# Kernel tuning notes

Measured on AMD Instinct MI355X. Metric: run time of the kernel, lower is better.

Reference implementation:

```python
import jax, jax.numpy as jnp
import numpy as np
import math

D = 128      # d_model == num_filters
L = 4        # num_conv_layers
K = 7        # kernel_size
H = 8        # num_heads
B, S = 64, 400


def setup_inputs() -> dict:
    key = jax.random.key(0)
    ks = jax.random.split(key, 24)
    s = 0.02
    inp = {}
    inp['x'] = jax.random.normal(ks[0], (B, S, D), dtype=jnp.float32)
    # per-conv-layer params (stacked over L)
    inp['ln_g'] = jnp.ones((L, D), jnp.float32)
    inp['ln_b'] = jnp.zeros((L, D), jnp.float32)
    inp['dw_w'] = jax.random.normal(ks[1], (L, D, D, K), dtype=jnp.float32) * s
    inp['dw_b'] = jnp.zeros((L, D), jnp.float32)
    inp['pw_w'] = jax.random.normal(ks[2], (L, D, D), dtype=jnp.float32) * s
    inp['pw_b'] = jnp.zeros((L, D), jnp.float32)
    # attention block
    inp['attln_g'] = jnp.ones((D,), jnp.float32)
    inp['attln_b'] = jnp.zeros((D,), jnp.float32)
    inp['wq'] = jax.random.normal(ks[3], (D, D), dtype=jnp.float32) * s
    inp['bq'] = jnp.zeros((D,), jnp.float32)
    inp['wk'] = jax.random.normal(ks[4], (D, D), dtype=jnp.float32) * s
    inp['bk'] = jnp.zeros((D,), jnp.float32)
    inp['wv'] = jax.random.normal(ks[5], (D, D), dtype=jnp.float32) * s
    inp['bv'] = jnp.zeros((D,), jnp.float32)
    inp['wp'] = jax.random.normal(ks[6], (D, D), dtype=jnp.float32) * s
    inp['bp'] = jnp.zeros((D,), jnp.float32)
    # ffn
    inp['ffnln_g'] = jnp.ones((D,), jnp.float32)
    inp['ffnln_b'] = jnp.zeros((D,), jnp.float32)
    inp['fc_w'] = jax.random.normal(ks[7], (D, D), dtype=jnp.float32) * s
    inp['fc_b'] = jnp.zeros((D,), jnp.float32)
    return inp


def _layernorm(x, g, b, eps=1e-5):
    mu = jnp.mean(x, axis=-1, keepdims=True)
    var = jnp.var(x, axis=-1, keepdims=True)
    return (x - mu) * jax.lax.rsqrt(var + eps) * g + b


def _pos_encoding(seq_len, channels, dtype):
    pos = jnp.arange(seq_len, dtype=dtype)                       # [S]
    freq = 1.0 / (10000.0 ** (jnp.arange(0, channels, 2, dtype=dtype) / channels))
    sin_inp = pos[:, None] * freq[None, :]                       # [S, C/2]
    return jnp.concatenate([jnp.sin(sin_inp), jnp.cos(sin_inp)], axis=-1)  # [S, C]


def _encoder_fwd(x, ln_g, ln_b, dw_w, dw_b, pw_w, pw_b,
                 attln_g, attln_b, wq, bq, wk, bk, wv, bv, wp, bp,
                 ffnln_g, ffnln_b, fc_w, fc_b):
    b, s, d = x.shape
    out = x + _pos_encoding(s, d, x.dtype)[None, :, :]

    # conv stack: LN -> transpose -> (full) conv K -> pointwise conv -> transpose
    pad = dw_w.shape[-1] // 2
    for i in range(dw_w.shape[0]):
        h = _layernorm(out, ln_g[i], ln_b[i])
        t = jnp.transpose(h, (0, 2, 1))                          # [B, D, S]
        t = jax.lax.conv_general_dilated(
            t, dw_w[i], window_strides=(1,), padding=[(pad, pad)],
            dimension_numbers=('NCH', 'OIH', 'NCH')) + dw_b[i][None, :, None]
        t = jnp.einsum('bds,fd->bfs', t, pw_w[i]) + pw_b[i][None, :, None]
        out = jnp.transpose(t, (0, 2, 1))                        # [B, S, D]

    # causal self-attention (explicit scores, per original)
    h = _layernorm(out, attln_g, attln_b)
    hd = d // H
    q = (jnp.einsum('bsd,od->bso', h, wq) + bq).reshape(b, s, H, hd)
    k = (jnp.einsum('bsd,od->bso', h, wk) + bk).reshape(b, s, H, hd)
    v = (jnp.einsum('bsd,od->bso', h, wv) + bv).reshape(b, s, H, hd)
    att = jnp.einsum('bqhd,bkhd->bhqk', q, k) / math.sqrt(hd)    # [B, H, S, S]
    causal = jnp.tril(jnp.ones((s, s), dtype=bool))
    att = jnp.where(causal[None, None], att, jnp.asarray(-1e10, att.dtype))
    att = jax.nn.softmax(att, axis=-1)
    y = jnp.einsum('bhqk,bkhd->bqhd', att, v).reshape(b, s, d)
    y = jnp.einsum('bsd,od->bso', y, wp) + bp

    # ffn
    y = _layernorm(y, ffnln_g, ffnln_b)
    y = jnp.einsum('bsd,od->bso', y, fc_w) + fc_b
    return jax.nn.relu(y)


def reference(x, ln_g, ln_b, dw_w, dw_b, pw_w, pw_b,
              attln_g, attln_b, wq, bq, wk, bk, wv, bv, wp, bp,
              ffnln_g, ffnln_b, fc_w, fc_b):
    return _encoder_fwd(x, ln_g, ln_b, dw_w, dw_b, pw_w, pw_b,
                        attln_g, attln_b, wq, bq, wk, bk, wv, bv, wp, bp,
                        ffnln_g, ffnln_b, fc_w, fc_b)
```

## Files before the change

kernel.cpp:

```cpp
#include <hip/hip_runtime.h>
#include <hip/hip_bf16.h>
#include <math.h>

#define Dm 128
#define Lc 4
#define Kc 7
#define Hh 8
#define Bb 64
#define Ss 400
#define SsP 448
#define TOK (Bb*Ss)

typedef __attribute__((ext_vector_type(8))) short bf16x8;
typedef __attribute__((ext_vector_type(4))) float f32x4;

__device__ __forceinline__ float bf2f(unsigned int u) {
    union { unsigned int i; float f; } x; x.i = u << 16; return x.f;
}
__device__ __forceinline__ unsigned short f2bf(float f) {
    __hip_bfloat16 h = __float2bfloat16(f);
    return __builtin_bit_cast(unsigned short, h);
}
__device__ __forceinline__ unsigned int packbf(float a, float b) {
    return (unsigned int)f2bf(a) | ((unsigned int)f2bf(b) << 16);
}


__global__ __launch_bounds__(256) void prep_all(const float* __restrict__ wq, const float* __restrict__ wk,
                                                const float* __restrict__ wv, const float* __restrict__ wp,
                                                const float* __restrict__ fc,
                                                const float* __restrict__ pw_w, const float* __restrict__ dw_w,
                                                const float* __restrict__ dw_b, const float* __restrict__ pw_b,
                                                float* __restrict__ pe, unsigned short* __restrict__ wf,
                                                float* __restrict__ mb, unsigned short* __restrict__ mwf) {
    __shared__ unsigned short hiS[64][136];
    __shared__ unsigned short loS[64][136];
    int blk = blockIdx.x;
    int tid = threadIdx.x;
    if (blk < 200) {
        int s = blk * 2 + (tid >> 7);
        int c = tid & 127;
        int j = (c < 64) ? c : (c - 64);
        float freq = expf(-(2.0f * j / 128.0f) * 9.210340371976184f);
        float a = (float)s * freq;
        pe[s * Dm + c] = (c < 64) ? sinf(a) : cosf(a);
        return;
    }
    if (blk < 520) {
        int idx = (blk - 200) * 256 + tid;
        int m = idx >> 14;
        int r = idx & 16383;
        int fragi = r >> 9, lr = (r >> 3) & 63, j = r & 7;
        int kb = fragi >> 3, nb = fragi & 7;
        int o = nb * 16 + (lr & 15);
        int d = kb * 32 + (lr >> 4) * 8 + j;
        const float* src = (m == 0) ? wq : (m == 1) ? wk : (m == 2) ? wv : (m == 3) ? wp : fc;
        wf[idx] = f2bf(src[o * Dm + d]);
        return;
    }
    if (blk < 524) {
        int l = blk - 520;
        int f = tid;
        if (f < Dm) {
            const float* pwl = pw_w + ((size_t)l * Dm + f) * Dm;
            const float* db  = dw_b + l * Dm;
            float acc = pw_b[l * Dm + f];
            #pragma unroll 8
            for (int c4 = 0; c4 < 32; ++c4) {
                float4 p = *(const float4*)(pwl + c4 * 4);
                float4 d = *(const float4*)(db + c4 * 4);
                acc += p.x * d.x + p.y * d.y + p.z * d.z + p.w * d.w;
            }
            mb[l * Dm + f] = acc;
        }
        return;
    }
    int mblk = blk - 524;
    int ih = mblk & 1;
    int k  = (mblk >> 1) % 7;
    int l  = mblk / 14;
    int lane = tid & 63, w = tid >> 6;

    const float* dwl = dw_w + (size_t)l * (Dm * Dm * Kc) + k;
    for (int it = 0; it < 32; ++it) {
        int idx = it * 256 + tid;
        int c = idx >> 6, il = idx & 63;
        int i = ih * 64 + il;
        float x = dwl[(size_t)(c * Dm + i) * Kc];
        unsigned short hi = f2bf(x);
        float lo = x - bf2f(hi);
        hiS[il][c] = hi;
        loS[il][c] = f2bf(lo);
    }
    __syncthreads();

    const float* pwl = pw_w + (size_t)l * Dm * Dm;
    int arow = lane & 15, ac = (lane >> 4) * 8;
    f32x4 acc[2][4];
    #pragma unroll
    for (int n = 0; n < 2; ++n)
        #pragma unroll
        for (int m = 0; m < 4; ++m) acc[n][m] = (f32x4){0.f, 0.f, 0.f, 0.f};

    #pragma unroll
    for (int kb = 0; kb < 4; ++kb) {
        int c0 = kb * 32 + ac;
        bf16x8 Bhi[2], Blo[2];
        #pragma unroll
        for (int n = 0; n < 2; ++n) {
            int f = (w * 2 + n) * 16 + arow;
            const float* rp = pwl + (size_t)f * Dm + c0;
            float4 a = *(const float4*)rp;
            float4 b = *(const float4*)(rp + 4);
            float v[8] = {a.x, a.y, a.z, a.w, b.x, b.y, b.z, b.w};
            unsigned short hh[8], ll[8];
            #pragma unroll
            for (int j = 0; j < 8; ++j) {
                hh[j] = f2bf(v[j]);
                ll[j] = f2bf(v[j] - bf2f(hh[j]));
            }
            uint4 uh = make_uint4((unsigned)hh[0] | ((unsigned)hh[1] << 16),
                                  (unsigned)hh[2] | ((unsigned)hh[3] << 16),
                                  (unsigned)hh[4] | ((unsigned)hh[5] << 16),
                                  (unsigned)hh[6] | ((unsigned)hh[7] << 16));
            uint4 ul = make_uint4((unsigned)ll[0] | ((unsigned)ll[1] << 16),
                                  (unsigned)ll[2] | ((unsigned)ll[3] << 16),
                                  (unsigned)ll[4] | ((unsigned)ll[5] << 16),
                                  (unsigned)ll[6] | ((unsigned)ll[7] << 16));
            Bhi[n] = __builtin_bit_cast(bf16x8, uh);
            Blo[n] = __builtin_bit_cast(bf16x8, ul);
        }
        #pragma unroll
        for (int m = 0; m < 4; ++m) {
            bf16x8 ahi = *(const bf16x8*)&hiS[m * 16 + arow][c0];
            bf16x8 alo = *(const bf16x8*)&loS[m * 16 + arow][c0];
            #pragma unroll
            for (int n = 0; n < 2; ++n) {
                acc[n][m] = __builtin_amdgcn_mfma_f32_16x16x32_bf16(ahi, Bhi[n], acc[n][m], 0, 0, 0);
                acc[n][m] = __builtin_amdgcn_mfma_f32_16x16x32_bf16(ahi, Blo[n], acc[n][m], 0, 0, 0);
                acc[n][m] = __builtin_amdgcn_mfma_f32_16x16x32_bf16(alo, Bhi[n], acc[n][m], 0, 0, 0);
            }
        }
    }
    #pragma unroll
    for (int n = 0; n < 2; ++n) {
        int nb = w * 2 + n;
        #pragma unroll
        for (int m = 0; m < 4; ++m) {
            int i0 = ih * 64 + m * 16 + (lane >> 4) * 4;
            int ib = i0 >> 5, i32 = i0 & 31;
            int lanep = ((i32 >> 3) << 4) | arow;
            int jb = i32 & 7;
            size_t frag = ((size_t)(l * 28 + (k * 4 + ib)) * 8 + nb);
            *(uint2*)(mwf + frag * 512 + lanep * 8 + jb) =
                make_uint2(packbf(acc[n][m][0], acc[n][m][1]),
                           packbf(acc[n][m][2], acc[n][m][3]));
        }
    }
}


__device__ __forceinline__ uint4 ln_core(float v[8],
                                         const float* __restrict__ g,
                                         const float* __restrict__ b, int c16) {
    float sum = 0.f, sq = 0.f;
    #pragma unroll
    for (int j = 0; j < 8; ++j) { sum += v[j]; sq += v[j] * v[j]; }
    #pragma unroll
    for (int off = 8; off; off >>= 1) {
        sum += __shfl_xor(sum, off);
        sq  += __shfl_xor(sq, off);
    }
    float mu = sum * (1.0f / 128.0f);
    float var = sq * (1.0f / 128.0f) - mu * mu;
    float rs = rsqrtf(var + 1e-5f);
    float4 g0 = *(const float4*)(g + c16 * 8);
    float4 g1 = *(const float4*)(g + c16 * 8 + 4);
    float4 b0 = *(const float4*)(b + c16 * 8);
    float4 b1 = *(const float4*)(b + c16 * 8 + 4);
    uint4 o;
    o.x = packbf((v[0] - mu) * rs * g0.x + b0.x, (v[1] - mu) * rs * g0.y + b0.y);
    o.y = packbf((v[2] - mu) * rs * g0.z + b0.z, (v[3] - mu) * rs * g0.w + b0.w);
    o.z = packbf((v[4] - mu) * rs * g1.x + b1.x, (v[5] - mu) * rs * g1.y + b1.y);
    o.w = packbf((v[6] - mu) * rs * g1.z + b1.z, (v[7] - mu) * rs * g1.w + b1.w);
    return o;
}

__device__ __forceinline__ uint4 ln_pack_bf(const unsigned short* __restrict__ rp,
                                            const float* __restrict__ g,
                                            const float* __restrict__ b, int c16) {
    uint4 u = *(const uint4*)rp;
    float v[8] = { bf2f(u.x & 0xffffu), bf2f(u.x >> 16), bf2f(u.y & 0xffffu), bf2f(u.y >> 16),
                   bf2f(u.z & 0xffffu), bf2f(u.z >> 16), bf2f(u.w & 0xffffu), bf2f(u.w >> 16) };
    return ln_core(v, g, b, c16);
}


__global__ __launch_bounds__(512) void conv_mfma(const unsigned short* __restrict__ in16,
                                                 const float* __restrict__ in32,
                                                 const float* __restrict__ pe,
                                                 const unsigned short* __restrict__ mwf,
                                                 const float* __restrict__ mb,
                                                 const float* __restrict__ lng,
                                                 const float* __restrict__ lnb,
                                                 unsigned short* __restrict__ out) {
    __shared__ unsigned short hs[54][136];
    int tid = threadIdx.x;
    int lane = tid & 63, w = tid >> 6;
    int bI = blockIdx.x / 9;
    int st = blockIdx.x % 9;
    int s0 = st * 48;
    for (int c = tid; c < 54 * 16; c += 512) {
        int row = c >> 4, c16 = c & 15;
        int gs = s0 - 3 + row;
        uint4 o = make_uint4(0u, 0u, 0u, 0u);
        if (gs >= 0 && gs < Ss) {
            if (in32) {
                const float* rp = in32 + ((size_t)bI * Ss + gs) * Dm + c16 * 8;
                const float* pp = pe + (size_t)gs * Dm + c16 * 8;
                float v[8];
                #pragma unroll
                for (int j = 0; j < 8; ++j) v[j] = rp[j] + pp[j];
                o = ln_core(v, lng, lnb, c16);
            } else {
                o = ln_pack_bf(in16 + ((size_t)bI * Ss + gs) * Dm + c16 * 8, lng, lnb, c16);
            }
        }
        *(uint4*)&hs[row][c16 * 8] = o;
    }
    __syncthreads();

    f32x4 acc[3];
    #pragma unroll
    for (int m = 0; m < 3; ++m) acc[m] = (f32x4){0.f, 0.f, 0.f, 0.f};

    int nb = w;
    int arow = lane & 15, acol = (lane >> 4) * 8;
    #pragma unroll 4
    for (int kb = 0; kb < 28; ++kb) {
        int k = kb >> 2, i0 = (kb & 3) * 32;
        bf16x8 bfr = *(const bf16x8*)(mwf + ((size_t)(kb * 8 + nb)) * 512 + lane * 8);
        #pragma unroll
        for (int m = 0; m < 3; ++m) {
            bf16x8 af = *(const bf16x8*)&hs[m * 16 + arow + k][i0 + acol];
            acc[m] = __builtin_amdgcn_mfma_f32_16x16x32_bf16(af, bfr, acc[m], 0, 0, 0);
        }
    }
    int rr = (lane >> 4) * 4;
    int f0 = nb * 16;
    float bias = mb[f0 + arow];
    #pragma unroll
    for (int m = 0; m < 3; ++m)
        #pragma unroll
        for (int r = 0; r < 4; ++r) {
            int s = s0 + m * 16 + rr + r;
            if (s < Ss)
                out[((size_t)bI * Ss + s) * Dm + f0 + arow] = f2bf(acc[m][r] + bias);
        }
}


__global__ __launch_bounds__(256) void qkv_mfma(const unsigned short* __restrict__ in,
                                                const float* __restrict__ lng,
                                                const float* __restrict__ lnb,
                                                const unsigned short* __restrict__ wfb,
                                                const float* __restrict__ bq,
                                                const float* __restrict__ bk,
                                                const float* __restrict__ bv,
                                                unsigned short* __restrict__ Qo,
                                                unsigned short* __restrict__ Ko,
                                                unsigned short* __restrict__ Vo) {
    __shared__ unsigned short hs[80][136];
    int tid = threadIdx.x;
    int lane = tid & 63, w = tid >> 6;
    int y = blockIdx.y;
    int bI = blockIdx.x / 5;
    int sb = (blockIdx.x % 5) * 80;
    const unsigned short* ib = in + ((size_t)bI * Ss + sb) * Dm;
    for (int c = tid; c < 80 * 16; c += 256) {
        int row = c >> 4, c16 = c & 15;
        *(uint4*)&hs[row][c16 * 8] = ln_pack_bf(ib + (size_t)row * Dm + c16 * 8, lng, lnb, c16);
    }
    __syncthreads();

    int nb0 = w * 2;
    int arow = lane & 15, acol = (lane >> 4) * 8;
    int nmat = (y == 0) ? 2 : 1;
    for (int mi = 0; mi < nmat; ++mi) {
        int mat = (y == 0) ? mi : 2;
        const unsigned short* wf = wfb + (size_t)mat * 16384;
        f32x4 acc[2][5];
        #pragma unroll
        for (int n = 0; n < 2; ++n)
            #pragma unroll
            for (int m = 0; m < 5; ++m) acc[n][m] = (f32x4){0.f, 0.f, 0.f, 0.f};
        #pragma unroll
        for (int kb = 0; kb < 4; ++kb) {
            bf16x8 b0 = *(const bf16x8*)(wf + ((size_t)(kb * 8 + nb0)) * 512 + lane * 8);
            bf16x8 b1 = *(const bf16x8*)(wf + ((size_t)(kb * 8 + nb0 + 1)) * 512 + lane * 8);
            #pragma unroll
            for (int m = 0; m < 5; ++m) {
                bf16x8 af = *(const bf16x8*)&hs[m * 16 + arow][kb * 32 + acol];
                acc[0][m] = __builtin_amdgcn_mfma_f32_16x16x32_bf16(af, b0, acc[0][m], 0, 0, 0);
                acc[1][m] = __builtin_amdgcn_mfma_f32_16x16x32_bf16(af, b1, acc[1][m], 0, 0, 0);
            }
        }
        int rr = (lane >> 4) * 4;
        const float* bias = (mat == 0) ? bq : (mat == 1) ? bk : bv;
        float sc = (mat == 0) ? 0.25f : 1.0f;
        #pragma unroll
        for (int n = 0; n < 2; ++n) {
            int hI = nb0 + n;
            float bvv = bias[hI * 16 + arow];
            if (mat < 2) {
                unsigned short* qo = (mat == 0) ? Qo : Ko;
                #pragma unroll
                for (int m = 0; m < 5; ++m)
                    #pragma unroll
                    for (int r = 0; r < 4; ++r) {
                        int s = sb + m * 16 + rr + r;
                        qo[(((size_t)(bI * Hh + hI)) * Ss + s) * 16 + arow] = f2bf((acc[n][m][r] + bvv) * sc);
                    }
            } else {
                unsigned short* base = Vo + ((size_t)(bI * Hh + hI) * 16 + arow) * SsP + sb;
                #pragma unroll
                for (int m = 0; m < 5; ++m) {
                    unsigned lo = packbf(acc[n][m][0] + bvv, acc[n][m][1] + bvv);
                    unsigned hi = packbf(acc[n][m][2] + bvv, acc[n][m][3] + bvv);
                    *(uint2*)(base + m * 16 + rr) = make_uint2(lo, hi);
                }
            }
        }
    }
}


__global__ __launch_bounds__(256) void gemm2(const unsigned short* __restrict__ in,
                                             const unsigned short* __restrict__ wf,
                                             const float* __restrict__ bias,
                                             const float* __restrict__ lng,
                                             const float* __restrict__ lnb,
                                             void* __restrict__ outv, int mode) {
    __shared__ unsigned short hs[80][136];
    int tid = threadIdx.x;
    int lane = tid & 63, w = tid >> 6;
    size_t tok0 = (size_t)blockIdx.x * 80;
    const unsigned short* ib = in + tok0 * Dm;
    if (lng) {
        for (int c = tid; c < 80 * 16; c += 256) {
            int row = c >> 4, c16 = c & 15;
            *(uint4*)&hs[row][c16 * 8] = ln_pack_bf(ib + (size_t)row * Dm + c16 * 8, lng, lnb, c16);
        }
    } else {
        for (int c = tid; c < 80 * 16; c += 256) {
            int row = c >> 4, c16 = c & 15;
            *(uint4*)&hs[row][c16 * 8] = *(const uint4*)(ib + (size_t)row * Dm + c16 * 8);
        }
    }
    __syncthreads();

    f32x4 acc[2][5];
    #pragma unroll
    for (int n = 0; n < 2; ++n)
        #pragma unroll
        for (int m = 0; m < 5; ++m) acc[n][m] = (f32x4){0.f, 0.f, 0.f, 0.f};

    int nb0 = w * 2;
    int arow = lane & 15, acol = (lane >> 4) * 8;
    #pragma unroll
    for (int kb = 0; kb < 4; ++kb) {
        bf16x8 b0 = *(const bf16x8*)(wf + ((size_t)(kb * 8 + nb0)) * 512 + lane * 8);
        bf16x8 b1 = *(const bf16x8*)(wf + ((size_t)(kb * 8 + nb0 + 1)) * 512 + lane * 8);
        #pragma unroll
        for (int m = 0; m < 5; ++m) {
            bf16x8 af = *(const bf16x8*)&hs[m * 16 + arow][kb * 32 + acol];
            acc[0][m] = __builtin_amdgcn_mfma_f32_16x16x32_bf16(af, b0, acc[0][m], 0, 0, 0);
            acc[1][m] = __builtin_amdgcn_mfma_f32_16x16x32_bf16(af, b1, acc[1][m], 0, 0, 0);
        }
    }
    int rr = (lane >> 4) * 4;
    #pragma unroll
    for (int n = 0; n < 2; ++n) {
        int f0 = (nb0 + n) * 16;
        float bvv = bias[f0 + arow];
        #pragma unroll
        for (int m = 0; m < 5; ++m)
            #pragma unroll
            for (int r = 0; r < 4; ++r) {
                float v = acc[n][m][r] + bvv;
                if (mode == 1) {
                    ((float*)outv)[(tok0 + m * 16 + rr + r) * Dm + f0 + arow] = fmaxf(v, 0.f);
                } else {
                    ((unsigned short*)outv)[(tok0 + m * 16 + rr + r) * Dm + f0 + arow] = f2bf(v);
                }
            }
    }
}


__global__ __launch_bounds__(320) void attn_mfma(const unsigned short* __restrict__ Q,
                                                 const unsigned short* __restrict__ Kb,
                                                 const unsigned short* __restrict__ VT,
                                                 unsigned short* __restrict__ out) {
    int wid = threadIdx.x >> 6, lane = threadIdx.x & 63;
    int bh = blockIdx.x;
    int qt = blockIdx.y * 5 + wid;
    int q15 = lane & 15, h = lane >> 4;
    int qg = qt * 16 + q15;

    uint4 qv = make_uint4(0u, 0u, 0u, 0u);
    if (h < 2) qv = *(const uint4*)(Q + ((size_t)bh * Ss + qg) * 16 + h * 8);
    bf16x8 qf = __builtin_bit_cast(bf16x8, qv);

    f32x4 o = (f32x4){0.f, 0.f, 0.f, 0.f};
    float mrow = -1e30f, lrow = 0.f;
    const unsigned short* kbase = Kb + (size_t)bh * Ss * 16;
    const unsigned short* vbase = VT + ((size_t)bh * 16 + q15) * SsP;
    int srcA = q15 + ((h & 1) << 5);
    int srcB = srcA + 16;
    bool t1 = h >= 2;
    f32x4 z = (f32x4){0.f, 0.f, 0.f, 0.f};

    for (int kt0 = 0; kt0 <= qt; kt0 += 4) {
        uint4 kv[4];
        #pragma unroll
        for (int t = 0; t < 4; ++t) {
            kv[t] = make_uint4(0u, 0u, 0u, 0u);
            if (h < 2 && kt0 + t <= qt)
                kv[t] = *(const uint4*)(kbase + (size_t)((kt0 + t) * 16 + q15) * 16 + h * 8);
        }
        f32x4 s[4];
        #pragma unroll
        for (int t = 0; t < 4; ++t)
            s[t] = __builtin_amdgcn_mfma_f32_16x16x32_bf16(__builtin_bit_cast(bf16x8, kv[t]), qf, z, 0, 0, 0);

        float p[16];
        #pragma unroll
        for (int t = 0; t < 4; ++t)
            #pragma unroll
            for (int r = 0; r < 4; ++r) {
                int ka = (kt0 + t) * 16 + h * 4 + r;
                p[t * 4 + r] = (ka <= qg) ? s[t][r] : -1e30f;
            }
        float tm = p[0];
        #pragma unroll
        for (int i = 1; i < 16; ++i) tm = fmaxf(tm, p[i]);
        tm = fmaxf(tm, __shfl_xor(tm, 16));
        tm = fmaxf(tm, __shfl_xor(tm, 32));
        float mnew = fmaxf(mrow, tm);
        float corr = __expf(mrow - mnew);
        float psum = 0.f;
        #pragma unroll
        for (int i = 0; i < 16; ++i) { p[i] = __expf(p[i] - mnew); psum += p[i]; }
        psum += __shfl_xor(psum, 16);
        psum += __shfl_xor(psum, 32);
        lrow = lrow * corr + psum;
        mrow = mnew;
        o[0] *= corr; o[1] *= corr; o[2] *= corr; o[3] *= corr;

        #pragma unroll
        for (int pr = 0; pr < 2; ++pr) {
            const float* pp = p + pr * 8;
            unsigned pk0 = packbf(pp[0], pp[1]), pk1 = packbf(pp[2], pp[3]);
            unsigned pk2 = packbf(pp[4], pp[5]), pk3 = packbf(pp[6], pp[7]);
            unsigned a0 = __shfl(pk0, srcA), a1 = __shfl(pk1, srcA);
            unsigned a2 = __shfl(pk0, srcB), a3 = __shfl(pk1, srcB);
            unsigned b0 = __shfl(pk2, srcA), b1 = __shfl(pk3, srcA);
            unsigned b2 = __shfl(pk2, srcB), b3 = __shfl(pk3, srcB);
            uint4 pw = make_uint4(t1 ? b0 : a0, t1 ? b1 : a1, t1 ? b2 : a2, t1 ? b3 : a3);
            uint4 vv = *(const uint4*)(vbase + (kt0 + pr * 2) * 16 + h * 8);
            o = __builtin_amdgcn_mfma_f32_16x16x32_bf16(__builtin_bit_cast(bf16x8, vv),
                                                        __builtin_bit_cast(bf16x8, pw), o, 0, 0, 0);
        }
    }
    float inv = 1.0f / lrow;
    int bI = bh >> 3, hh = bh & 7;
    unsigned short* op = out + ((size_t)bI * Ss + qg) * Dm + hh * 16 + h * 4;
    *(uint2*)op = make_uint2(packbf(o[0] * inv, o[1] * inv),
                             packbf(o[2] * inv, o[3] * inv));
}


extern "C" void kernel_launch(void* const* d_in, const int* in_sizes, int n_in,
                              void* d_out, int out_size, void* d_ws, size_t ws_size,
                              hipStream_t stream) {
    (void)in_sizes; (void)n_in; (void)out_size; (void)ws_size;
    const float* x       = (const float*)d_in[0];
    const float* ln_g    = (const float*)d_in[1];
    const float* ln_b    = (const float*)d_in[2];
    const float* dw_w    = (const float*)d_in[3];
    const float* dw_b    = (const float*)d_in[4];
    const float* pw_w    = (const float*)d_in[5];
    const float* pw_b    = (const float*)d_in[6];
    const float* attln_g = (const float*)d_in[7];
    const float* attln_b = (const float*)d_in[8];
    const float* wq = (const float*)d_in[9];
    const float* bq = (const float*)d_in[10];
    const float* wk = (const float*)d_in[11];
    const float* bk = (const float*)d_in[12];
    const float* wv = (const float*)d_in[13];
    const float* bv = (const float*)d_in[14];
    const float* wp = (const float*)d_in[15];
    const float* bp = (const float*)d_in[16];
    const float* ffnln_g = (const float*)d_in[17];
    const float* ffnln_b = (const float*)d_in[18];
    const float* fc_w = (const float*)d_in[19];
    const float* fc_b = (const float*)d_in[20];

    float* ws = (float*)d_ws;
    float* pe = ws;
    float* mb = pe + 51200;
    unsigned short* mwf = (unsigned short*)(mb + 512);
    unsigned short* wfb = mwf + 458752;
    unsigned short* C1  = wfb + 81920;
    unsigned short* C2  = C1 + 3276800;
    unsigned short* Qb  = C2 + 3276800;
    unsigned short* Kb2 = Qb + 3276800;
    unsigned short* VTb = Kb2 + 3276800;
    unsigned short* A1b = VTb + 3670016;

    prep_all<<<580, 256, 0, stream>>>(wq, wk, wv, wp, fc_w, pw_w, dw_w, dw_b, pw_b,
                                      pe, wfb, mb, mwf);

    conv_mfma<<<Bb * 9, 512, 0, stream>>>(nullptr, x, pe, mwf,              mb,          ln_g,          ln_b,          C1);
    conv_mfma<<<Bb * 9, 512, 0, stream>>>(C1, nullptr, nullptr, mwf + 114688,     mb + Dm,     ln_g + Dm,     ln_b + Dm,     C2);
    conv_mfma<<<Bb * 9, 512, 0, stream>>>(C2, nullptr, nullptr, mwf + 2 * 114688, mb + 2 * Dm, ln_g + 2 * Dm, ln_b + 2 * Dm, C1);
    conv_mfma<<<Bb * 9, 512, 0, stream>>>(C1, nullptr, nullptr, mwf + 3 * 114688, mb + 3 * Dm, ln_g + 3 * Dm, ln_b + 3 * Dm, C2);

    qkv_mfma<<<dim3(320, 2), 256, 0, stream>>>(C2, attln_g, attln_b, wfb, bq, bk, bv, Qb, Kb2, VTb);
    attn_mfma<<<dim3(512, 5), 320, 0, stream>>>(Qb, Kb2, VTb, A1b);
    gemm2<<<320, 256, 0, stream>>>(A1b, wfb + 3 * 16384, bp, nullptr, nullptr, C1, 0);

    gemm2<<<320, 256, 0, stream>>>(C1, wfb + 4 * 16384, fc_b, ffnln_g, ffnln_b, d_out, 1);
}
```

Before: 122.7 us.

## Fuse four conv layers and QKV projection into one halo-tiled kernel

Replaces the four per-layer conv kernels and the QKV kernel with a single kernel. Each block loads an 80-token tile plus a 12-token halo on each side, runs all four convolution layers in shared memory with the valid range shrinking per layer, then applies the attention layernorm and the Q/K/V projections. This removes four intermediate activation round-trips through global memory and four launches. In exchange it recomputes halo tokens, launches only 320 blocks with larger shared memory use, and cannot overlap the layer boundaries across blocks.

```diff
diff --git a/kernel.cpp b/kernel.cpp
--- a/kernel.cpp
+++ b/kernel.cpp
@@ -196,116 +196,134 @@
 }
 
 
-__global__ __launch_bounds__(512) void conv_mfma(const unsigned short* __restrict__ in16,
-                                                 const float* __restrict__ in32,
-                                                 const float* __restrict__ pe,
-                                                 const unsigned short* __restrict__ mwf,
-                                                 const float* __restrict__ mb,
-                                                 const float* __restrict__ lng,
-                                                 const float* __restrict__ lnb,
-                                                 unsigned short* __restrict__ out) {
-    __shared__ unsigned short hs[54][136];
-    int tid = threadIdx.x;
-    int lane = tid & 63, w = tid >> 6;
-    int bI = blockIdx.x / 9;
-    int st = blockIdx.x % 9;
-    int s0 = st * 48;
-    for (int c = tid; c < 54 * 16; c += 512) {
-        int row = c >> 4, c16 = c & 15;
-        int gs = s0 - 3 + row;
+__global__ __launch_bounds__(512) void mega(const float* __restrict__ x,
+                                            const float* __restrict__ pe,
+                                            const unsigned short* __restrict__ mwf,
+                                            const float* __restrict__ mb,
+                                            const float* __restrict__ ln_g,
+                                            const float* __restrict__ ln_b,
+                                            const float* __restrict__ attg,
+                                            const float* __restrict__ attb,
+                                            const unsigned short* __restrict__ wfb,
+                                            const float* __restrict__ bq,
+                                            const float* __restrict__ bk,
+                                            const float* __restrict__ bv,
+                                            unsigned short* __restrict__ Qo,
+                                            unsigned short* __restrict__ Ko,
+                                            unsigned short* __restrict__ Vo) {
+    __shared__ unsigned short L[118][136];
+    __shared__ unsigned short R[101][128];
+    int tid = threadIdx.x, lane = tid & 63, w = tid >> 6;
+    int bI = blockIdx.x / 5;
+    int s0 = (blockIdx.x % 5) * 80;
+    int arow = lane & 15, acol = (lane >> 4) * 8, rr = (lane >> 4) * 4;
+    int nb0 = (w & 3) * 2, mh = w >> 2;
+
+    for (int c = tid; c < 118 * 16; c += 512) {
+        int idx = c >> 4, c16 = c & 15;
+        int g = s0 - 12 + idx;
         uint4 o = make_uint4(0u, 0u, 0u, 0u);
-        if (gs >= 0 && gs < Ss) {
-            if (in32) {
-                const float* rp = in32 + ((size_t)bI * Ss + gs) * Dm + c16 * 8;
-                const float* pp = pe + (size_t)gs * Dm + c16 * 8;
-                float v[8];
-                #pragma unroll
-                for (int j = 0; j < 8; ++j) v[j] = rp[j] + pp[j];
-                o = ln_core(v, lng, lnb, c16);
-            } else {
-                o = ln_pack_bf(in16 + ((size_t)bI * Ss + gs) * Dm + c16 * 8, lng, lnb, c16);
-            }
-        }
-        *(uint4*)&hs[row][c16 * 8] = o;
+        if (g >= 0 && g < Ss) {
+            const float* rp = x + ((size_t)bI * Ss + g) * Dm + c16 * 8;
+            const float* pp = pe + (size_t)g * Dm + c16 * 8;
+            float v[8];
+            #pragma unroll
+            for (int j = 0; j < 8; ++j) v[j] = rp[j] + pp[j];
+            o = ln_core(v, ln_g, ln_b, c16);
+        }
+        *(uint4*)&L[idx][c16 * 8] = o;
     }
     __syncthreads();
 
-    f32x4 acc[3];
-    #pragma unroll
-    for (int m = 0; m < 3; ++m) acc[m] = (f32x4){0.f, 0.f, 0.f, 0.f};
-
-    int nb = w;
-    int arow = lane & 15, acol = (lane >> 4) * 8;
-    #pragma unroll 4
-    for (int kb = 0; kb < 28; ++kb) {
-        int k = kb >> 2, i0 = (kb & 3) * 32;
-        bf16x8 bfr = *(const bf16x8*)(mwf + ((size_t)(kb * 8 + nb)) * 512 + lane * 8);
-        #pragma unroll
-        for (int m = 0; m < 3; ++m) {
-            bf16x8 af = *(const bf16x8*)&hs[m * 16 + arow + k][i0 + acol];
-            acc[m] = __builtin_amdgcn_mfma_f32_16x16x32_bf16(af, bfr, acc[m], 0, 0, 0);
-        }
-    }
-    int rr = (lane >> 4) * 4;
-    int f0 = nb * 16;
-    float bias = mb[f0 + arow];
-    #pragma unroll
-    for (int m = 0; m < 3; ++m)
-        #pragma unroll
-        for (int r = 0; r < 4; ++r) {
-            int s = s0 + m * 16 + rr + r;
-            if (s < Ss)
-                out[((size_t)bI * Ss + s) * Dm + f0 + arow] = f2bf(acc[m][r] + bias);
-        }
-}
-
-
-__global__ __launch_bounds__(256) void qkv_mfma(const unsigned short* __restrict__ in,
-                                                const float* __restrict__ lng,
-                                                const float* __restrict__ lnb,
-                                                const unsigned short* __restrict__ wfb,
-                                                const float* __restrict__ bq,
-                                                const float* __restrict__ bk,
-                                                const float* __restrict__ bv,
-                                                unsigned short* __restrict__ Qo,
-                                                unsigned short* __restrict__ Ko,
-                                                unsigned short* __restrict__ Vo) {
-    __shared__ unsigned short hs[80][136];
-    int tid = threadIdx.x;
-    int lane = tid & 63, w = tid >> 6;
-    int y = blockIdx.y;
-    int bI = blockIdx.x / 5;
-    int sb = (blockIdx.x % 5) * 80;
-    const unsigned short* ib = in + ((size_t)bI * Ss + sb) * Dm;
-    for (int c = tid; c < 80 * 16; c += 256) {
-        int row = c >> 4, c16 = c & 15;
-        *(uint4*)&hs[row][c16 * 8] = ln_pack_bf(ib + (size_t)row * Dm + c16 * 8, lng, lnb, c16);
-    }
-    __syncthreads();
-
-    int nb0 = w * 2;
-    int arow = lane & 15, acol = (lane >> 4) * 8;
-    int nmat = (y == 0) ? 2 : 1;
-    for (int mi = 0; mi < nmat; ++mi) {
-        int mat = (y == 0) ? mi : 2;
+    const int NT[4] = {7, 6, 6, 5};
+    for (int l = 0; l < 4; ++l) {
+        int in_lo = 3 * l;
+        int out_lo = 3 * (l + 1), out_hi = 104 - 3 * (l + 1);
+        int ntiles = NT[l];
+        const unsigned short* mw = mwf + (size_t)l * 114688;
+
+        f32x4 acc[2][4];
+        #pragma unroll
+        for (int n = 0; n < 2; ++n)
+            #pragma unroll
+            for (int mi = 0; mi < 4; ++mi) acc[n][mi] = (f32x4){0.f, 0.f, 0.f, 0.f};
+
+        #pragma unroll 4
+        for (int kb = 0; kb < 28; ++kb) {
+            int k = kb >> 2, i0 = (kb & 3) * 32;
+            bf16x8 b0 = *(const bf16x8*)(mw + ((size_t)(kb * 8 + nb0)) * 512 + lane * 8);
+            bf16x8 b1 = *(const bf16x8*)(mw + ((size_t)(kb * 8 + nb0 + 1)) * 512 + lane * 8);
+            #pragma unroll
+            for (int mi = 0; mi < 4; ++mi) {
+                int m = mh + 2 * mi;
+                if (m < ntiles) {
+                    bf16x8 af = *(const bf16x8*)&L[in_lo + m * 16 + arow + k][i0 + acol];
+                    acc[0][mi] = __builtin_amdgcn_mfma_f32_16x16x32_bf16(af, b0, acc[0][mi], 0, 0, 0);
+                    acc[1][mi] = __builtin_amdgcn_mfma_f32_16x16x32_bf16(af, b1, acc[1][mi], 0, 0, 0);
+                }
+            }
+        }
+        __syncthreads();
+        #pragma unroll
+        for (int n = 0; n < 2; ++n) {
+            int f = (nb0 + n) * 16 + arow;
+            float bias = mb[l * Dm + f];
+            #pragma unroll
+            for (int mi = 0; mi < 4; ++mi) {
+                int m = mh + 2 * mi;
+                if (m < ntiles) {
+                    #pragma unroll
+                    for (int r = 0; r < 4; ++r) {
+                        int o = out_lo + m * 16 + rr + r;
+                        if (o < out_hi) R[o][f] = f2bf(acc[n][mi][r] + bias);
+                    }
+                }
+            }
+        }
+        __syncthreads();
+
+        if (l < 3) {
+            const float* lg = ln_g + (l + 1) * Dm;
+            const float* lb = ln_b + (l + 1) * Dm;
+            int span = out_hi - out_lo;
+            for (int c = tid; c < span * 16; c += 512) {
+                int idx = out_lo + (c >> 4), c16 = c & 15;
+                int g = s0 - 12 + idx;
+                uint4 o = make_uint4(0u, 0u, 0u, 0u);
+                if (g >= 0 && g < Ss)
+                    o = ln_pack_bf(&R[idx][c16 * 8], lg, lb, c16);
+                *(uint4*)&L[idx][c16 * 8] = o;
+            }
+        } else {
+            for (int c = tid; c < 80 * 16; c += 512) {
+                int idx = 12 + (c >> 4), c16 = c & 15;
+                *(uint4*)&L[idx][c16 * 8] = ln_pack_bf(&R[idx][c16 * 8], attg, attb, c16);
+            }
+        }
+        __syncthreads();
+    }
+
+    for (int mat = 0; mat < 3; ++mat) {
         const unsigned short* wf = wfb + (size_t)mat * 16384;
-        f32x4 acc[2][5];
+        f32x4 acc[2][3];
         #pragma unroll
         for (int n = 0; n < 2; ++n)
             #pragma unroll
-            for (int m = 0; m < 5; ++m) acc[n][m] = (f32x4){0.f, 0.f, 0.f, 0.f};
+            for (int mi = 0; mi < 3; ++mi) acc[n][mi] = (f32x4){0.f, 0.f, 0.f, 0.f};
         #pragma unroll
         for (int kb = 0; kb < 4; ++kb) {
             bf16x8 b0 = *(const bf16x8*)(wf + ((size_t)(kb * 8 + nb0)) * 512 + lane * 8);
             bf16x8 b1 = *(const bf16x8*)(wf + ((size_t)(kb * 8 + nb0 + 1)) * 512 + lane * 8);
             #pragma unroll
-            for (int m = 0; m < 5; ++m) {
-                bf16x8 af = *(const bf16x8*)&hs[m * 16 + arow][kb * 32 + acol];
-                acc[0][m] = __builtin_amdgcn_mfma_f32_16x16x32_bf16(af, b0, acc[0][m], 0, 0, 0);
-                acc[1][m] = __builtin_amdgcn_mfma_f32_16x16x32_bf16(af, b1, acc[1][m], 0, 0, 0);
-            }
-        }
-        int rr = (lane >> 4) * 4;
+            for (int mi = 0; mi < 3; ++mi) {
+                int m = mh + 2 * mi;
+                if (m < 5) {
+                    bf16x8 af = *(const bf16x8*)&L[12 + m * 16 + arow][kb * 32 + acol];
+                    acc[0][mi] = __builtin_amdgcn_mfma_f32_16x16x32_bf16(af, b0, acc[0][mi], 0, 0, 0);
+                    acc[1][mi] = __builtin_amdgcn_mfma_f32_16x16x32_bf16(af, b1, acc[1][mi], 0, 0, 0);
+                }
+            }
+        }
         const float* bias = (mat == 0) ? bq : (mat == 1) ? bk : bv;
         float sc = (mat == 0) ? 0.25f : 1.0f;
         #pragma unroll
@@ -315,19 +333,27 @@
             if (mat < 2) {
                 unsigned short* qo = (mat == 0) ? Qo : Ko;
                 #pragma unroll
-                for (int m = 0; m < 5; ++m)
-                    #pragma unroll
-                    for (int r = 0; r < 4; ++r) {
-                        int s = sb + m * 16 + rr + r;
-                        qo[(((size_t)(bI * Hh + hI)) * Ss + s) * 16 + arow] = f2bf((acc[n][m][r] + bvv) * sc);
+                for (int mi = 0; mi < 3; ++mi) {
+                    int m = mh + 2 * mi;
+                    if (m < 5) {
+                        #pragma unroll
+                        for (int r = 0; r < 4; ++r) {
+                            int s = s0 + m * 16 + rr + r;
+                            qo[(((size_t)(bI * Hh + hI)) * Ss + s) * 16 + arow] =
+                                f2bf((acc[n][mi][r] + bvv) * sc);
+                        }
                     }
+                }
             } else {
-                unsigned short* base = Vo + ((size_t)(bI * Hh + hI) * 16 + arow) * SsP + sb;
+                unsigned short* base = Vo + ((size_t)(bI * Hh + hI) * 16 + arow) * SsP + s0;
                 #pragma unroll
-                for (int m = 0; m < 5; ++m) {
-                    unsigned lo = packbf(acc[n][m][0] + bvv, acc[n][m][1] + bvv);
-                    unsigned hi = packbf(acc[n][m][2] + bvv, acc[n][m][3] + bvv);
-                    *(uint2*)(base + m * 16 + rr) = make_uint2(lo, hi);
+                for (int mi = 0; mi < 3; ++mi) {
+                    int m = mh + 2 * mi;
+                    if (m < 5) {
+                        unsigned lo = packbf(acc[n][mi][0] + bvv, acc[n][mi][1] + bvv);
+                        unsigned hi = packbf(acc[n][mi][2] + bvv, acc[n][mi][3] + bvv);
+                        *(uint2*)(base + m * 16 + rr) = make_uint2(lo, hi);
+                    }
                 }
             }
         }
@@ -512,22 +538,18 @@
     float* mb = pe + 51200;
     unsigned short* mwf = (unsigned short*)(mb + 512);
     unsigned short* wfb = mwf + 458752;
-    unsigned short* C1  = wfb + 81920;
-    unsigned short* C2  = C1 + 3276800;
-    unsigned short* Qb  = C2 + 3276800;
+    unsigned short* Qb  = wfb + 81920;
     unsigned short* Kb2 = Qb + 3276800;
     unsigned short* VTb = Kb2 + 3276800;
     unsigned short* A1b = VTb + 3670016;
+    unsigned short* C1  = A1b + 3276800;
 
     prep_all<<<580, 256, 0, stream>>>(wq, wk, wv, wp, fc_w, pw_w, dw_w, dw_b, pw_b,
                                       pe, wfb, mb, mwf);
 
-    conv_mfma<<<Bb * 9, 512, 0, stream>>>(nullptr, x, pe, mwf,              mb,          ln_g,          ln_b,          C1);
-    conv_mfma<<<Bb * 9, 512, 0, stream>>>(C1, nullptr, nullptr, mwf + 114688,     mb + Dm,     ln_g + Dm,     ln_b + Dm,     C2);
-    conv_mfma<<<Bb * 9, 512, 0, stream>>>(C2, nullptr, nullptr, mwf + 2 * 114688, mb + 2 * Dm, ln_g + 2 * Dm, ln_b + 2 * Dm, C1);
-    conv_mfma<<<Bb * 9, 512, 0, stream>>>(C1, nullptr, nullptr, mwf + 3 * 114688, mb + 3 * Dm, ln_g + 3 * Dm, ln_b + 3 * Dm, C2);
-
-    qkv_mfma<<<dim3(320, 2), 256, 0, stream>>>(C2, attln_g, attln_b, wfb, bq, bk, bv, Qb, Kb2, VTb);
+    mega<<<320, 512, 0, stream>>>(x, pe, mwf, mb, ln_g, ln_b, attln_g, attln_b,
+                                  wfb, bq, bk, bv, Qb, Kb2, VTb);
+
     attn_mfma<<<dim3(512, 5), 320, 0, stream>>>(Qb, Kb2, VTb, A1b);
     gemm2<<<320, 256, 0, stream>>>(A1b, wfb + 3 * 16384, bp, nullptr, nullptr, C1, 0);
 
```

Result: no change. 121.3 us (-1.1%).
